# Kernel optimization log

Hardware: AMD Instinct MI355X
Metric: run time of the kernel (lower is better)

Reference implementation:

```python
import jax, jax.numpy as jnp
import numpy as np

OBS = 256      # observation_space_size == state_vector_len
SV = 2047      # STATE_VECTORS = WMG_MAX_OBS
D = 256        # tfm_vec_size = 8 heads * 32 head_size
H = 8
HD = 32
L = 2          # TFM_NUM_LAYERS
FF = 1024      # TFM_HIDDEN_SIZE
ACH = 512      # AC_HIDDEN_LAYER_SIZE
A = 16         # action_space_size


def setup_inputs() -> dict:
    key = jax.random.key(0)
    ks = jax.random.split(key, 24)
    r = lambda k, s: (jax.random.normal(k, s, jnp.float32) * 0.02)
    inp = {
        "observation": jax.random.normal(ks[0], (OBS,), jnp.float32),
        "old_vectors": jax.random.normal(ks[1], (SV, OBS), jnp.float32),
        "W_core": r(ks[2], (OBS, D)), "b_core": jnp.zeros((D,), jnp.float32),
        # memo embedding takes cat(state_vec, age_onehot) of size OBS+SV
        "W_memo": r(ks[3], (OBS + SV, D)), "b_memo": jnp.zeros((D,), jnp.float32),
        "Wq": r(ks[4], (L, D, D)), "bq": jnp.zeros((L, D), jnp.float32),
        "Wk": r(ks[5], (L, D, D)), "bk": jnp.zeros((L, D), jnp.float32),
        "Wv": r(ks[6], (L, D, D)), "bv": jnp.zeros((L, D), jnp.float32),
        "Wo": r(ks[7], (L, D, D)), "bo": jnp.zeros((L, D), jnp.float32),
        "ln1_g": jnp.ones((L, D), jnp.float32), "ln1_b": jnp.zeros((L, D), jnp.float32),
        "ln2_g": jnp.ones((L, D), jnp.float32), "ln2_b": jnp.zeros((L, D), jnp.float32),
        "W_ff1": r(ks[8], (L, D, FF)), "b_ff1": jnp.zeros((L, FF), jnp.float32),
        "W_ff2": r(ks[9], (L, FF, D)), "b_ff2": jnp.zeros((L, D), jnp.float32),
        "aW1": r(ks[10], (D, ACH)), "ab1": jnp.zeros((ACH,), jnp.float32),
        "aW2": r(ks[11], (ACH, ACH)), "ab2": jnp.zeros((ACH,), jnp.float32),
        "aWo": r(ks[12], (ACH, A)), "abo": jnp.zeros((A,), jnp.float32),
        "cW1": r(ks[13], (D, ACH)), "cb1": jnp.zeros((ACH,), jnp.float32),
        "cW2": r(ks[14], (ACH, ACH)), "cb2": jnp.zeros((ACH,), jnp.float32),
        "cWo": r(ks[15], (ACH, 1)), "cbo": jnp.zeros((1,), jnp.float32),
    }
    return inp


def _ln(x, g, b, eps=1e-5):
    m = jnp.mean(x, axis=-1, keepdims=True)
    v = jnp.mean(jnp.square(x - m), axis=-1, keepdims=True)
    return (x - m) * jax.lax.rsqrt(v + eps) * g + b


def reference(observation, old_vectors, W_core, b_core, W_memo, b_memo,
              Wq, bq, Wk, bk, Wv, bv, Wo, bo,
              ln1_g, ln1_b, ln2_g, ln2_b, W_ff1, b_ff1, W_ff2, b_ff2,
              aW1, ab1, aW2, ab2, aWo, abo, cW1, cb1, cW2, cb2, cWo, cbo):
    # core embedding [D]
    emb0 = observation @ W_core + b_core
    # fused memo + age-onehot embedding: cat(vec_i, e_i) @ W_memo == vec_i @ W_memo[:OBS] + W_memo[OBS+i]
    memo_emb = old_vectors @ W_memo[:OBS] + W_memo[OBS:] + b_memo  # [SV, D]
    x = jnp.concatenate([emb0[None, :], memo_emb], axis=0)[None]   # [1, 1+SV, D]
    S = 1 + SV
    scale = 1.0 / np.sqrt(HD).astype(np.float32)
    for l in range(L):
        q = (x @ Wq[l] + bq[l]).reshape(1, S, H, HD)
        k = (x @ Wk[l] + bk[l]).reshape(1, S, H, HD)
        v = (x @ Wv[l] + bv[l]).reshape(1, S, H, HD)
        scores = jnp.einsum('bqhd,bkhd->bhqk', q, k) * scale       # [1,H,S,S]
        probs = jax.nn.softmax(scores, axis=-1)
        ctx = jnp.einsum('bhqk,bkhd->bqhd', probs, v).reshape(1, S, D)
        x = _ln(x + ctx @ Wo[l] + bo[l], ln1_g[l], ln1_b[l])
        h = jax.nn.gelu(x @ W_ff1[l] + b_ff1[l])
        x = _ln(x + h @ W_ff2[l] + b_ff2[l], ln2_g[l], ln2_b[l])
    t = x[:, 0, :]                                                 # [1, D]
    ha = jnp.tanh(jnp.tanh(t @ aW1 + ab1) @ aW2 + ab2)
    policy = ha @ aWo + abo                                        # [1, A] logits
    hc = jnp.tanh(jnp.tanh(t @ cW1 + cb1) @ cW2 + cb2)
    value_est = hc @ cWo + cbo                                     # [1, 1]
    # WMG_MAX_MEMOS == 0 path: new state vector is tanh(observation)
    new_vector = jnp.tanh(observation)                             # [OBS]
    return value_est, policy, new_vector
```

## Files before the change

kernel.cpp:

```cpp
#include <hip/hip_runtime.h>
#include <stdint.h>

typedef __attribute__((ext_vector_type(8))) short bf16x8;
typedef __attribute__((ext_vector_type(4))) float f32x4;

constexpr int kSEQ = 2048;
constexpr int kD   = 256;
constexpr int kHD  = 32;
constexpr int kFF  = 1024;
constexpr int kA   = 16;

__device__ __forceinline__ unsigned short f2b(float f) {
  union { float f; unsigned int u; } v; v.f = f;
  unsigned int r = v.u + 0x7FFFu + ((v.u >> 16) & 1u);
  return (unsigned short)(r >> 16);
}

struct ConvTable {
  const float* src[13];
  int K[13];
  int N[13];
  int dst[13];
  int tstart[14];
};

union SharedU {
  struct { unsigned short lt[64][72]; } cv;
  struct { unsigned short Al[64][40]; unsigned short Bl[32][40]; } g64;
  struct { unsigned short Kl[64][40]; unsigned short Vt[32][72];
           unsigned short Pl[4][16][72]; } at;
  struct { unsigned short As[16][264]; float2 red[4][16]; } lg;
};

struct MegaParams {
  ConvTable tab;
  const float *obs, *oldv, *Wcore, *bcore, *Wmemo0, *bmemo, *Wmemo2;
  const float *bq, *bk, *bv, *bo, *ln1g, *ln1b, *ln2g, *ln2b, *bff1, *bff2;
  const float *aW1, *ab1, *aW2, *ab2, *aWo, *abo;
  const float *cW1, *cb1, *cW2, *cb2, *cWo, *cbo;
  float* xf; unsigned short* xb;
  unsigned short *qb, *kb, *vb, *hb, *wT;
  float *pacc, *pml, *pf, *h1, *h2, *out;
  int oQKV[2], oWoT[2], oFF1[2], oFF2[2];
  int convJobs, nsplit, tpb;
};

__device__ void conv_job(const MegaParams& p, SharedU& sh, int job) {
  const int tid = threadIdx.x;
  if (job == p.convJobs) {
    float a = p.bcore[tid];
    #pragma unroll 8
    for (int k = 0; k < 256; k++) a += p.obs[k] * p.Wcore[k * kD + tid];
    p.xf[tid] = a;
    p.xb[tid] = f2b(a);
    return;
  }
  int m = 0;
  while (job >= p.tab.tstart[m + 1]) m++;
  const int tloc = job - p.tab.tstart[m];
  const int N = p.tab.N[m], K = p.tab.K[m];
  const int ntile = N >> 6;
  const int k0 = (tloc / ntile) * 64, n0 = (tloc % ntile) * 64;
  const float* src = p.tab.src[m];
  {
    const int r = tid >> 2, c16 = (tid & 3) * 16;
    const float* sp = src + (size_t)(k0 + r) * N + n0 + c16;
    #pragma unroll
    for (int j = 0; j < 16; j++) sh.cv.lt[r][c16 + j] = f2b(sp[j]);
  }
  __syncthreads();
  {
    const int n = tid >> 2, kc = (tid & 3) * 16;
    unsigned short* dp = p.wT + p.tab.dst[m] + (size_t)(n0 + n) * K + k0 + kc;
    unsigned short g[16];
    #pragma unroll
    for (int j = 0; j < 16; j++) g[j] = sh.cv.lt[kc + j][n];
    *(bf16x8*)dp = *(bf16x8*)&g[0];
    *(bf16x8*)(dp + 8) = *(bf16x8*)&g[8];
  }
}

__device__ void memo_job(const MegaParams& p, SharedU& sh, int job) {
  const int tid = threadIdx.x;
  const int w = tid >> 6, l = tid & 63, lg = l >> 4, lr = l & 15;
  const int sr = tid >> 2, sk = (tid & 3) * 8;
  const int kr = tid >> 3, nc = (tid & 7) * 4;
  const int m0 = (job & 31) * 64, n0 = (job >> 5) * 32;
  f32x4 acc[2];
  #pragma unroll
  for (int c = 0; c < 2; c++)
    #pragma unroll
    for (int i = 0; i < 4; i++) acc[c][i] = 0.f;

  auto loadA = [&](int k0) -> bf16x8 {
    bf16x8 av;
    if (m0 + sr < 2047) {
      const float* ap = p.oldv + (size_t)(m0 + sr) * 256 + k0 + sk;
      #pragma unroll
      for (int j = 0; j < 8; j++) av[j] = (short)f2b(ap[j]);
    } else {
      #pragma unroll
      for (int j = 0; j < 8; j++) av[j] = 0;
    }
    return av;
  };
  auto loadB = [&](int k0, float* b4) {
    const float* bp = p.Wmemo0 + (size_t)(k0 + kr) * kD + n0 + nc;
    #pragma unroll
    for (int j = 0; j < 4; j++) b4[j] = bp[j];
  };

  bf16x8 av = loadA(0);
  float b4[4];
  loadB(0, b4);

  for (int k0 = 0; k0 < 256; k0 += 32) {
    __syncthreads();
    *(bf16x8*)&sh.g64.Al[sr][sk] = av;
    #pragma unroll
    for (int j = 0; j < 4; j++) sh.g64.Bl[nc + j][kr] = f2b(b4[j]);
    __syncthreads();
    if (k0 + 32 < 256) {
      av = loadA(k0 + 32);
      loadB(k0 + 32, b4);
    }
    bf16x8 af = *(bf16x8*)&sh.g64.Al[w * 16 + lr][8 * lg];
    #pragma unroll
    for (int c = 0; c < 2; c++) {
      bf16x8 bf = *(bf16x8*)&sh.g64.Bl[c * 16 + lr][8 * lg];
      acc[c] = __builtin_amdgcn_mfma_f32_16x16x32_bf16(af, bf, acc[c], 0, 0, 0);
    }
  }

  #pragma unroll
  for (int c = 0; c < 2; c++)
    #pragma unroll
    for (int i = 0; i < 4; i++) {
      const int gr = m0 + w * 16 + 4 * lg + i;
      const int gc = n0 + c * 16 + lr;
      if (gr >= 2047) continue;
      const float v = acc[c][i] + p.bmemo[gc] + p.Wmemo2[(size_t)gr * kD + gc];
      p.xf[(size_t)(gr + 1) * kD + gc] = v;
      p.xb[(size_t)(gr + 1) * kD + gc] = f2b(v);
    }
}

__global__ __launch_bounds__(256) void k_cvm(MegaParams p) {
  __shared__ SharedU sh;
  if (blockIdx.x < 256) memo_job(p, sh, blockIdx.x);
  else conv_job(p, sh, blockIdx.x - 256);
}

template <int EPI>
__device__ __forceinline__ void gemm_job(
    SharedU& sh, int m0, int n0, const unsigned short* Ap, int lda, int Kloop,
    const unsigned short* BT, int ldb,
    const float* p0, const float* p1, const float* p2,
    void* o0, void* o1, void* o2) {
  const int tid = threadIdx.x;
  const int w = tid >> 6, l = tid & 63, lg = l >> 4, lr = l & 15;
  const int sr = tid >> 2, sk = (tid & 3) * 8;
  f32x4 acc[2];
  #pragma unroll
  for (int c = 0; c < 2; c++)
    #pragma unroll
    for (int i = 0; i < 4; i++) acc[c][i] = 0.f;

  bf16x8 av = *(const bf16x8*)(Ap + (size_t)(m0 + sr) * lda + sk);
  bf16x8 bv;
  if (tid < 128) bv = *(const bf16x8*)(BT + (size_t)(n0 + sr) * ldb + sk);

  for (int k0 = 0; k0 < Kloop; k0 += 32) {
    __syncthreads();
    *(bf16x8*)&sh.g64.Al[sr][sk] = av;
    if (tid < 128) *(bf16x8*)&sh.g64.Bl[sr][sk] = bv;
    __syncthreads();
    if (k0 + 32 < Kloop) {
      av = *(const bf16x8*)(Ap + (size_t)(m0 + sr) * lda + k0 + 32 + sk);
      if (tid < 128)
        bv = *(const bf16x8*)(BT + (size_t)(n0 + sr) * ldb + k0 + 32 + sk);
    }
    bf16x8 af = *(bf16x8*)&sh.g64.Al[w * 16 + lr][8 * lg];
    #pragma unroll
    for (int c = 0; c < 2; c++) {
      bf16x8 bf = *(bf16x8*)&sh.g64.Bl[c * 16 + lr][8 * lg];
      acc[c] = __builtin_amdgcn_mfma_f32_16x16x32_bf16(af, bf, acc[c], 0, 0, 0);
    }
  }

  #pragma unroll
  for (int c = 0; c < 2; c++) {
    #pragma unroll
    for (int i = 0; i < 4; i++) {
      const int gr = m0 + w * 16 + 4 * lg + i;
      const int gc = n0 + c * 16 + lr;
      float v = acc[c][i];
      if constexpr (EPI == 1) {
        const int t = gc >> 8, cc = gc & 255;
        const float* bp = (t == 0) ? p0 : (t == 1 ? p1 : p2);
        unsigned short* op = (t == 0) ? (unsigned short*)o0
                              : (t == 1 ? (unsigned short*)o1
                                        : (unsigned short*)o2);
        v += bp[cc];
        if (t == 0) v *= 0.17677669529663687f;
        op[(size_t)gr * kD + cc] = f2b(v);
      } else if constexpr (EPI == 2) {
        v += p0[gc];
        const float u = 0.7978845608028654f * (v + 0.044715f * v * v * v);
        const float g = v / (1.0f + __expf(-2.0f * u));
        ((unsigned short*)o0)[(size_t)gr * kFF + gc] = f2b(g);
      } else {
        ((float*)o0)[(size_t)gr * kD + gc] = v;
      }
    }
  }
}

__global__ __launch_bounds__(256) void k_qkv(MegaParams p, int lyr) {
  __shared__ SharedU sh;
  const int job = blockIdx.x;
  const int m0 = (job & 31) * 64, n0 = (job >> 5) * 32;
  gemm_job<1>(sh, m0, n0, p.xb, 256, 256, p.wT + p.oQKV[lyr], 256,
              p.bq + lyr * 256, p.bk + lyr * 256, p.bv + lyr * 256,
              p.qb, p.kb, p.vb);
}

__global__ __launch_bounds__(256) void k_ff1(MegaParams p, int lyr) {
  __shared__ SharedU sh;
  const int job = blockIdx.x;
  const int m0 = (job & 31) * 64, n0 = (job >> 5) * 32;
  gemm_job<2>(sh, m0, n0, p.xb, 256, 256, p.wT + p.oFF1[lyr], 256,
              p.bff1 + lyr * 1024, nullptr, nullptr, p.hb, nullptr, nullptr);
}

__global__ __launch_bounds__(256) void k_ff2p(MegaParams p, int lyr) {
  __shared__ SharedU sh;
  const int job = blockIdx.x;
  const int m0 = (job & 31) * 64;
  const int n0 = ((job >> 5) & 7) * 32;
  const int kc = (job >> 8) * 256;
  gemm_job<3>(sh, m0, n0, p.hb + kc, kFF, 256,
              p.wT + p.oFF2[lyr] + kc, kFF, nullptr, nullptr, nullptr,
              p.pf + (size_t)(job >> 8) * kSEQ * kD, nullptr, nullptr);
}

__device__ void attn_job(SharedU& sh, int qb_, int h, int s, int tpb,
                         const unsigned short* q, const unsigned short* k,
                         const unsigned short* v, float* pacc, float* pml) {
  const int tid = threadIdx.x;
  const int w = tid >> 6, l = tid & 63, lg = l >> 4, lr = l & 15;
  const int q0 = qb_ * 64;
  const int hoff = h * kHD;
  const int sr = tid >> 2, sk = (tid & 3) * 8;
  const int t0 = s * tpb;

  const bf16x8 qf =
      *(const bf16x8*)(q + (size_t)(q0 + w * 16 + lr) * kD + hoff + 8 * lg);

  float m_[4], l_[4];
  f32x4 acc[2];
  #pragma unroll
  for (int i = 0; i < 4; i++) { m_[i] = -1e30f; l_[i] = 0.f; }
  #pragma unroll
  for (int dt = 0; dt < 2; dt++)
    #pragma unroll
    for (int i = 0; i < 4; i++) acc[dt][i] = 0.f;

  bf16x8 kreg = *(const bf16x8*)(k + (size_t)(t0 * 64 + sr) * kD + hoff + sk);
  bf16x8 vreg = *(const bf16x8*)(v + (size_t)(t0 * 64 + sr) * kD + hoff + sk);

  for (int t = 0; t < tpb; t++) {
    __syncthreads();
    *(bf16x8*)&sh.at.Kl[sr][sk] = kreg;
    #pragma unroll
    for (int j = 0; j < 8; j++) sh.at.Vt[sk + j][sr] = (unsigned short)vreg[j];
    __syncthreads();
    if (t + 1 < tpb) {
      const size_t nx = (size_t)((t0 + t + 1) * 64 + sr) * kD + hoff + sk;
      kreg = *(const bf16x8*)(k + nx);
      vreg = *(const bf16x8*)(v + nx);
    }
    f32x4 sc[4];
    #pragma unroll
    for (int c = 0; c < 4; c++) {
      f32x4 z;
      #pragma unroll
      for (int i = 0; i < 4; i++) z[i] = 0.f;
      bf16x8 kf = *(bf16x8*)&sh.at.Kl[c * 16 + lr][8 * lg];
      sc[c] = __builtin_amdgcn_mfma_f32_16x16x32_bf16(qf, kf, z, 0, 0, 0);
    }
    float tm[4];
    #pragma unroll
    for (int i = 0; i < 4; i++)
      tm[i] = fmaxf(fmaxf(sc[0][i], sc[1][i]), fmaxf(sc[2][i], sc[3][i]));
    #pragma unroll
    for (int mm = 1; mm <= 8; mm <<= 1)
      #pragma unroll
      for (int i = 0; i < 4; i++) tm[i] = fmaxf(tm[i], __shfl_xor(tm[i], mm));
    float pv[4][4], rs[4], corr[4];
    #pragma unroll
    for (int i = 0; i < 4; i++) {
      const float nm = fmaxf(m_[i], tm[i]);
      corr[i] = __expf(m_[i] - nm);
      m_[i] = nm;
      rs[i] = 0.f;
    }
    #pragma unroll
    for (int c = 0; c < 4; c++)
      #pragma unroll
      for (int i = 0; i < 4; i++) {
        pv[c][i] = __expf(sc[c][i] - m_[i]);
        rs[i] += pv[c][i];
      }
    #pragma unroll
    for (int mm = 1; mm <= 8; mm <<= 1)
      #pragma unroll
      for (int i = 0; i < 4; i++) rs[i] += __shfl_xor(rs[i], mm);
    #pragma unroll
    for (int i = 0; i < 4; i++) {
      l_[i] = l_[i] * corr[i] + rs[i];
      acc[0][i] *= corr[i];
      acc[1][i] *= corr[i];
    }
    #pragma unroll
    for (int c = 0; c < 4; c++)
      #pragma unroll
      for (int i = 0; i < 4; i++)
        sh.at.Pl[w][4 * lg + i][c * 16 + lr] = f2b(pv[c][i]);
    __syncthreads();
    #pragma unroll
    for (int k2 = 0; k2 < 2; k2++) {
      bf16x8 pf_ = *(bf16x8*)&sh.at.Pl[w][lr][k2 * 32 + 8 * lg];
      #pragma unroll
      for (int dt = 0; dt < 2; dt++) {
        bf16x8 vf = *(bf16x8*)&sh.at.Vt[dt * 16 + lr][k2 * 32 + 8 * lg];
        acc[dt] = __builtin_amdgcn_mfma_f32_16x16x32_bf16(pf_, vf, acc[dt], 0, 0, 0);
      }
    }
  }

  const int pb = s * 8 + h;
  float* pa = pacc + (size_t)pb * kSEQ * kHD;
  float* pm = pml + (size_t)pb * kSEQ * 2;
  #pragma unroll
  for (int dt = 0; dt < 2; dt++)
    #pragma unroll
    for (int i = 0; i < 4; i++) {
      const int gr = q0 + w * 16 + 4 * lg + i;
      pa[(size_t)gr * kHD + dt * 16 + lr] = acc[dt][i];
    }
  if (lr == 0) {
    #pragma unroll
    for (int i = 0; i < 4; i++) {
      const int gr = q0 + w * 16 + 4 * lg + i;
      float2 ml; ml.x = m_[i]; ml.y = l_[i];
      *(float2*)&pm[(size_t)gr * 2] = ml;
    }
  }
}

__global__ __launch_bounds__(256) void k_attn(MegaParams p) {
  __shared__ SharedU sh;
  const int job = blockIdx.x;
  const int qb_ = job & 31, h = (job >> 5) & 7, s = job >> 8;
  attn_job(sh, qb_, h, s, p.tpb, p.qb, p.kb, p.vb, p.pacc, p.pml);
}

__device__ __forceinline__ void ln_write(SharedU& sh, float vloc[4][4], int r0,
                                         const float* gam, const float* bet,
                                         float* xf, unsigned short* xb) {
  const int tid = threadIdx.x;
  const int w = tid >> 6, l = tid & 63, lg = l >> 4, lr = l & 15;
  float ps[4], ps2[4];
  #pragma unroll
  for (int i = 0; i < 4; i++) {
    ps[i] = 0.f; ps2[i] = 0.f;
    #pragma unroll
    for (int c = 0; c < 4; c++) {
      ps[i] += vloc[c][i];
      ps2[i] += vloc[c][i] * vloc[c][i];
    }
  }
  #pragma unroll
  for (int mm = 1; mm <= 8; mm <<= 1)
    #pragma unroll
    for (int i = 0; i < 4; i++) {
      ps[i] += __shfl_xor(ps[i], mm);
      ps2[i] += __shfl_xor(ps2[i], mm);
    }
  if (lr == 0) {
    #pragma unroll
    for (int i = 0; i < 4; i++) {
      float2 t; t.x = ps[i]; t.y = ps2[i];
      sh.lg.red[w][4 * lg + i] = t;
    }
  }
  __syncthreads();
  #pragma unroll
  for (int i = 0; i < 4; i++) {
    const int ri = 4 * lg + i;
    float sx = 0.f, sx2 = 0.f;
    #pragma unroll
    for (int ww = 0; ww < 4; ww++) {
      float2 t = sh.lg.red[ww][ri];
      sx += t.x; sx2 += t.y;
    }
    const float mean = sx * (1.0f / 256.0f);
    const float var = sx2 * (1.0f / 256.0f) - mean * mean;
    const float rstd = rsqrtf(var + 1e-5f);
    const int gr = r0 + ri;
    #pragma unroll
    for (int c = 0; c < 4; c++) {
      const int col = w * 64 + c * 16 + lr;
      const float y = (vloc[c][i] - mean) * rstd * gam[col] + bet[col];
      xf[(size_t)gr * kD + col] = y;
      xb[(size_t)gr * kD + col] = f2b(y);
    }
  }
}

__global__ __launch_bounds__(256) void k_woln(MegaParams p, int lyr) {
  __shared__ SharedU sh;
  const unsigned short* BT = p.wT + p.oWoT[lyr];
  const float* bias = p.bo + lyr * kD;
  const float* gam = p.ln1g + lyr * kD;
  const float* bet = p.ln1b + lyr * kD;
  const int tid = threadIdx.x;
  const int w = tid >> 6, l = tid & 63, lg = l >> 4, lr = l & 15;
  const int r0 = blockIdx.x * 16;
  {
    const int row = r0 + (tid >> 4);
    const int kc = (tid & 15) * 16;
    const int h_ = kc >> 5;
    float mx = -1e30f;
    for (int s2 = 0; s2 < p.nsplit; s2++)
      mx = fmaxf(mx, p.pml[((size_t)(s2 * 8 + h_) * kSEQ + row) * 2]);
    float L = 0.f;
    const int d0 = kc & 31;
    float o[16];
    #pragma unroll
    for (int j = 0; j < 16; j++) o[j] = 0.f;
    for (int s2 = 0; s2 < p.nsplit; s2++) {
      const size_t pb = (size_t)(s2 * 8 + h_) * kSEQ + row;
      const float2 t = *(const float2*)&p.pml[pb * 2];
      const float es = __expf(t.x - mx);
      L += t.y * es;
      const float* pa = p.pacc + pb * kHD + d0;
      #pragma unroll
      for (int j = 0; j < 16; j++) o[j] += pa[j] * es;
    }
    const float inv = 1.0f / L;
    unsigned short* dst = &sh.lg.As[tid >> 4][kc];
    #pragma unroll
    for (int j = 0; j < 16; j++) dst[j] = f2b(o[j] * inv);
  }
  __syncthreads();
  f32x4 acc[4];
  #pragma unroll
  for (int c = 0; c < 4; c++)
    #pragma unroll
    for (int i = 0; i < 4; i++) acc[c][i] = 0.f;
  #pragma unroll 2
  for (int k0 = 0; k0 < 256; k0 += 32) {
    bf16x8 af = *(bf16x8*)&sh.lg.As[lr][k0 + 8 * lg];
    #pragma unroll
    for (int c = 0; c < 4; c++) {
      bf16x8 bf = *(const bf16x8*)(BT + (size_t)(w * 64 + c * 16 + lr) * 256 +
                                   k0 + 8 * lg);
      acc[c] = __builtin_amdgcn_mfma_f32_16x16x32_bf16(af, bf, acc[c], 0, 0, 0);
    }
  }
  float vloc[4][4];
  #pragma unroll
  for (int c = 0; c < 4; c++)
    #pragma unroll
    for (int i = 0; i < 4; i++) {
      const int col = w * 64 + c * 16 + lr;
      const int gr = r0 + 4 * lg + i;
      vloc[c][i] = acc[c][i] + bias[col] + p.xf[(size_t)gr * kD + col];
    }
  ln_write(sh, vloc, r0, gam, bet, p.xf, p.xb);
}

__global__ __launch_bounds__(256) void k_ln2r(MegaParams p, int lyr) {
  const float* bias = p.bff2 + lyr * kD;
  const float* gam = p.ln2g + lyr * kD;
  const float* bet = p.ln2b + lyr * kD;
  const int w = threadIdx.x >> 6, l = threadIdx.x & 63;
  const int row = blockIdx.x * 4 + w;
  f32x4 v = *(const f32x4*)(p.xf + (size_t)row * kD + l * 4);
  f32x4 b4 = *(const f32x4*)(bias + l * 4);
  #pragma unroll
  for (int i = 0; i < 4; i++) v[i] += b4[i];
  #pragma unroll
  for (int s = 0; s < 4; s++) {
    f32x4 t = *(const f32x4*)(p.pf + ((size_t)s * kSEQ + row) * kD + l * 4);
    #pragma unroll
    for (int i = 0; i < 4; i++) v[i] += t[i];
  }
  float su = v[0] + v[1] + v[2] + v[3];
  #pragma unroll
  for (int mm = 1; mm < 64; mm <<= 1) su += __shfl_xor(su, mm);
  const float mn = su * (1.0f / 256.0f);
  const float d0 = v[0] - mn, d1 = v[1] - mn, d2 = v[2] - mn, d3 = v[3] - mn;
  float s2 = d0 * d0 + d1 * d1 + d2 * d2 + d3 * d3;
  #pragma unroll
  for (int mm = 1; mm < 64; mm <<= 1) s2 += __shfl_xor(s2, mm);
  const float rstd = rsqrtf(s2 * (1.0f / 256.0f) + 1e-5f);
  f32x4 g4 = *(const f32x4*)(gam + l * 4);
  f32x4 be4 = *(const f32x4*)(bet + l * 4);
  f32x4 y;
  y[0] = d0 * rstd * g4[0] + be4[0];
  y[1] = d1 * rstd * g4[1] + be4[1];
  y[2] = d2 * rstd * g4[2] + be4[2];
  y[3] = d3 * rstd * g4[3] + be4[3];
  *(f32x4*)(p.xf + (size_t)row * kD + l * 4) = y;
  unsigned long long pk = (unsigned long long)f2b(y[0]) |
                          ((unsigned long long)f2b(y[1]) << 16) |
                          ((unsigned long long)f2b(y[2]) << 32) |
                          ((unsigned long long)f2b(y[3]) << 48);
  *(unsigned long long*)(p.xb + (size_t)row * kD + l * 4) = pk;
}

__global__ __launch_bounds__(256) void k_h1(MegaParams p) {
  __shared__ float tl[256];
  __shared__ float red[4][64];
  const int tid = threadIdx.x;
  tl[tid] = p.xf[tid];
  __syncthreads();
  const int jj = blockIdx.x * 64;
  const bool actor = jj < 512;
  const float* W = actor ? p.aW1 : p.cW1;
  const float* b = actor ? p.ab1 : p.cb1;
  const int j0 = actor ? jj : jj - 512;
  const int ks = tid >> 6, j = tid & 63;
  float s = 0.f;
  #pragma unroll 4
  for (int k2 = ks * 64; k2 < ks * 64 + 64; k2++)
    s += tl[k2] * W[(size_t)k2 * 512 + j0 + j];
  red[ks][j] = s;
  __syncthreads();
  if (tid < 64) {
    float t = red[0][tid] + red[1][tid] + red[2][tid] + red[3][tid] + b[j0 + tid];
    p.h1[jj + tid] = tanhf(t);
  }
}

__global__ __launch_bounds__(256) void k_h2(MegaParams p) {
  __shared__ float tl[512];
  __shared__ float red[4][64];
  const int tid = threadIdx.x;
  const int jj = blockIdx.x * 64;
  const bool actor = jj < 512;
  const float* hin = actor ? p.h1 : p.h1 + 512;
  tl[tid] = hin[tid];
  tl[tid + 256] = hin[tid + 256];
  __syncthreads();
  const float* W = actor ? p.aW2 : p.cW2;
  const float* b = actor ? p.ab2 : p.cb2;
  const int j0 = actor ? jj : jj - 512;
  const int ks = tid >> 6, j = tid & 63;
  float s = 0.f;
  #pragma unroll 4
  for (int k2 = ks * 128; k2 < ks * 128 + 128; k2++)
    s += tl[k2] * W[(size_t)k2 * 512 + j0 + j];
  red[ks][j] = s;
  __syncthreads();
  if (tid < 64) {
    float t = red[0][tid] + red[1][tid] + red[2][tid] + red[3][tid] + b[j0 + tid];
    p.h2[jj + tid] = tanhf(t);
  }
}

__global__ __launch_bounds__(256) void k_h3(MegaParams p) {
  __shared__ float ha[512], hc[512], vred[4];
  const int tid = threadIdx.x;
  ha[tid] = p.h2[tid];
  ha[tid + 256] = p.h2[tid + 256];
  hc[tid] = p.h2[512 + tid];
  hc[tid + 256] = p.h2[768 + tid];
  __syncthreads();
  const int g = tid >> 4, l16 = tid & 15;
  float s = 0.f;
  for (int k2 = l16 * 32; k2 < l16 * 32 + 32; k2++)
    s += ha[k2] * p.aWo[(size_t)k2 * kA + g];
  #pragma unroll
  for (int mm = 1; mm <= 8; mm <<= 1) s += __shfl_xor(s, mm);
  if (l16 == 0) p.out[1 + g] = s + p.abo[g];
  float vv = hc[tid] * p.cWo[tid] + hc[tid + 256] * p.cWo[tid + 256];
  #pragma unroll
  for (int mm = 1; mm <= 32; mm <<= 1) vv += __shfl_xor(vv, mm);
  if ((tid & 63) == 0) vred[tid >> 6] = vv;
  __syncthreads();
  if (tid == 0)
    p.out[0] = vred[0] + vred[1] + vred[2] + vred[3] + p.cbo[0];
  p.out[17 + tid] = tanhf(p.obs[tid]);
}

extern "C" void kernel_launch(void* const* d_in, const int* in_sizes, int n_in,
                              void* d_out, int out_size, void* d_ws, size_t ws_size,
                              hipStream_t stream) {
  const float* obs   = (const float*)d_in[0];
  const float* oldv  = (const float*)d_in[1];
  const float* Wcore = (const float*)d_in[2];
  const float* bcore = (const float*)d_in[3];
  const float* Wmemo = (const float*)d_in[4];
  const float* bmemo = (const float*)d_in[5];
  const float* Wq    = (const float*)d_in[6];
  const float* bq    = (const float*)d_in[7];
  const float* Wk    = (const float*)d_in[8];
  const float* bk    = (const float*)d_in[9];
  const float* Wv    = (const float*)d_in[10];
  const float* bv    = (const float*)d_in[11];
  const float* Wo    = (const float*)d_in[12];
  const float* bo    = (const float*)d_in[13];
  const float* ln1g  = (const float*)d_in[14];
  const float* ln1b  = (const float*)d_in[15];
  const float* ln2g  = (const float*)d_in[16];
  const float* ln2b  = (const float*)d_in[17];
  const float* Wff1  = (const float*)d_in[18];
  const float* bff1  = (const float*)d_in[19];
  const float* Wff2  = (const float*)d_in[20];
  const float* bff2  = (const float*)d_in[21];

  MegaParams P;
  P.obs = obs; P.oldv = oldv; P.Wcore = Wcore; P.bcore = bcore;
  P.Wmemo0 = Wmemo; P.bmemo = bmemo; P.Wmemo2 = Wmemo + 256 * 256;
  P.bq = bq; P.bk = bk; P.bv = bv; P.bo = bo;
  P.ln1g = ln1g; P.ln1b = ln1b; P.ln2g = ln2g; P.ln2b = ln2b;
  P.bff1 = bff1; P.bff2 = bff2;
  P.aW1 = (const float*)d_in[22]; P.ab1 = (const float*)d_in[23];
  P.aW2 = (const float*)d_in[24]; P.ab2 = (const float*)d_in[25];
  P.aWo = (const float*)d_in[26]; P.abo = (const float*)d_in[27];
  P.cW1 = (const float*)d_in[28]; P.cb1 = (const float*)d_in[29];
  P.cW2 = (const float*)d_in[30]; P.cb2 = (const float*)d_in[31];
  P.cWo = (const float*)d_in[32]; P.cbo = (const float*)d_in[33];

  char* ws = (char*)d_ws;
  P.xf = (float*)(ws + 0);
  P.xb = (unsigned short*)(ws + (2u << 20));
  P.qb = (unsigned short*)(ws + (3u << 20));
  P.kb = (unsigned short*)(ws + (4u << 20));
  P.vb = (unsigned short*)(ws + (5u << 20));
  P.hb = (unsigned short*)(ws + (6u << 20));
  P.wT = (unsigned short*)(ws + (10u << 20));
  P.out = (float*)d_out;

  int nsplit = 8;
  const size_t paccOff = (size_t)14u << 20;
  const size_t pmlOff  = (size_t)31u << 20;
  const size_t pfOff   = (size_t)33u << 20;
  while (nsplit > 1 &&
         (paccOff + (size_t)nsplit * 8 * kSEQ * kHD * 4 > pmlOff ||
          pfOff + (size_t)4 * kSEQ * kD * 4 + 16384 > ws_size))
    nsplit >>= 1;
  P.pacc = (float*)(ws + paccOff);
  P.pml  = (float*)(ws + pmlOff);
  P.pf   = (float*)(ws + pfOff);
  P.h1 = (float*)(ws + pfOff + (size_t)4 * kSEQ * kD * 4);
  P.h2 = P.h1 + 1024;
  P.nsplit = nsplit;
  P.tpb = 32 / nsplit;

  int cur = 0;
  for (int l2 = 0; l2 < 2; l2++) {
    P.oQKV[l2] = cur; cur += 196608;
    P.oWoT[l2] = cur; cur += 65536;
    P.oFF1[l2] = cur; cur += 262144;
    P.oFF2[l2] = cur; cur += 262144;
  }

  int idx = 0, ts = 0;
  auto add = [&](const float* s, int K, int N, int dst) {
    P.tab.src[idx] = s; P.tab.K[idx] = K; P.tab.N[idx] = N;
    P.tab.dst[idx] = dst; P.tab.tstart[idx] = ts;
    ts += (K >> 6) * (N >> 6); idx++;
  };
  for (int l2 = 0; l2 < 2; l2++) {
    add(Wq + l2 * 65536, 256, 256, P.oQKV[l2]);
    add(Wk + l2 * 65536, 256, 256, P.oQKV[l2] + 65536);
    add(Wv + l2 * 65536, 256, 256, P.oQKV[l2] + 131072);
    add(Wo + l2 * 65536, 256, 256, P.oWoT[l2]);
    add(Wff1 + l2 * 262144, 256, 1024, P.oFF1[l2]);
    add(Wff2 + l2 * 262144, 1024, 256, P.oFF2[l2]);
  }
  P.tab.tstart[idx] = ts;
  P.convJobs = ts;

  k_cvm<<<256 + ts + 1, 256, 0, stream>>>(P);
  for (int lyr = 0; lyr < 2; lyr++) {
    k_qkv<<<768, 256, 0, stream>>>(P, lyr);
    k_attn<<<256 * nsplit, 256, 0, stream>>>(P);
    k_woln<<<128, 256, 0, stream>>>(P, lyr);
    k_ff1<<<1024, 256, 0, stream>>>(P, lyr);
    k_ff2p<<<1024, 256, 0, stream>>>(P, lyr);
    k_ln2r<<<512, 256, 0, stream>>>(P, lyr);
  }
  k_h1<<<16, 256, 0, stream>>>(P);
  k_h2<<<16, 256, 0, stream>>>(P);
  k_h3<<<1, 256, 0, stream>>>(P);
}
```

Measured before the change: 190.3 us.

## Fuse FF2 GEMM with residual LayerNorm and merge actor-critic hidden layers

Replaces the split-K FF2 GEMM, which wrote four fp32 partial buffers, and the separate LN2 reduction kernel with a single kernel. Each block stages a 16-row slice of the FF1 activations in LDS, runs the full K=1024 MFMA, adds the bias and residual, and applies LayerNorm in place. This removes the partial-sum global round trip and one launch per layer. The cost is that each block now does a long serial K loop and only 128 blocks are launched, which lowers parallelism. The actor/critic first and second MLP layers are also merged into one kernel, with each block recomputing the first layer redundantly, to save a launch.

```diff
diff --git a/kernel.cpp b/kernel.cpp
--- a/kernel.cpp
+++ b/kernel.cpp
@@ -40,7 +40,7 @@
   const float *cW1, *cb1, *cW2, *cb2, *cWo, *cbo;
   float* xf; unsigned short* xb;
   unsigned short *qb, *kb, *vb, *hb, *wT;
-  float *pacc, *pml, *pf, *h1, *h2, *out;
+  float *pacc, *pml, *h2, *out;
   int oQKV[2], oWoT[2], oFF1[2], oFF2[2];
   int convJobs, nsplit, tpb;
 };
@@ -204,13 +204,11 @@
         v += bp[cc];
         if (t == 0) v *= 0.17677669529663687f;
         op[(size_t)gr * kD + cc] = f2b(v);
-      } else if constexpr (EPI == 2) {
+      } else {
         v += p0[gc];
         const float u = 0.7978845608028654f * (v + 0.044715f * v * v * v);
         const float g = v / (1.0f + __expf(-2.0f * u));
         ((unsigned short*)o0)[(size_t)gr * kFF + gc] = f2b(g);
-      } else {
-        ((float*)o0)[(size_t)gr * kD + gc] = v;
       }
     }
   }
@@ -233,17 +231,6 @@
               p.bff1 + lyr * 1024, nullptr, nullptr, p.hb, nullptr, nullptr);
 }
 
-__global__ __launch_bounds__(256) void k_ff2p(MegaParams p, int lyr) {
-  __shared__ SharedU sh;
-  const int job = blockIdx.x;
-  const int m0 = (job & 31) * 64;
-  const int n0 = ((job >> 5) & 7) * 32;
-  const int kc = (job >> 8) * 256;
-  gemm_job<3>(sh, m0, n0, p.hb + kc, kFF, 256,
-              p.wT + p.oFF2[lyr] + kc, kFF, nullptr, nullptr, nullptr,
-              p.pf + (size_t)(job >> 8) * kSEQ * kD, nullptr, nullptr);
-}
-
 __device__ void attn_job(SharedU& sh, int qb_, int h, int s, int tpb,
                          const unsigned short* q, const unsigned short* k,
                          const unsigned short* v, float* pacc, float* pml) {
@@ -366,9 +353,10 @@
   attn_job(sh, qb_, h, s, p.tpb, p.qb, p.kb, p.vb, p.pacc, p.pml);
 }
 
-__device__ __forceinline__ void ln_write(SharedU& sh, float vloc[4][4], int r0,
-                                         const float* gam, const float* bet,
-                                         float* xf, unsigned short* xb) {
+__device__ __forceinline__ void ln_write(float2 (*red)[16], float vloc[4][4],
+                                         int r0, const float* gam,
+                                         const float* bet, float* xf,
+                                         unsigned short* xb) {
   const int tid = threadIdx.x;
   const int w = tid >> 6, l = tid & 63, lg = l >> 4, lr = l & 15;
   float ps[4], ps2[4];
@@ -392,7 +380,7 @@
     #pragma unroll
     for (int i = 0; i < 4; i++) {
       float2 t; t.x = ps[i]; t.y = ps2[i];
-      sh.lg.red[w][4 * lg + i] = t;
+      red[w][4 * lg + i] = t;
     }
   }
   __syncthreads();
@@ -402,7 +390,7 @@
     float sx = 0.f, sx2 = 0.f;
     #pragma unroll
     for (int ww = 0; ww < 4; ww++) {
-      float2 t = sh.lg.red[ww][ri];
+      float2 t = red[ww][ri];
       sx += t.x; sx2 += t.y;
     }
     const float mean = sx * (1.0f / 256.0f);
@@ -420,7 +408,8 @@
 }
 
 __global__ __launch_bounds__(256) void k_woln(MegaParams p, int lyr) {
-  __shared__ SharedU sh;
+  __shared__ unsigned short As[16][264];
+  __shared__ float2 red[4][16];
   const unsigned short* BT = p.wT + p.oWoT[lyr];
   const float* bias = p.bo + lyr * kD;
   const float* gam = p.ln1g + lyr * kD;
@@ -450,7 +439,7 @@
       for (int j = 0; j < 16; j++) o[j] += pa[j] * es;
     }
     const float inv = 1.0f / L;
-    unsigned short* dst = &sh.lg.As[tid >> 4][kc];
+    unsigned short* dst = &As[tid >> 4][kc];
     #pragma unroll
     for (int j = 0; j < 16; j++) dst[j] = f2b(o[j] * inv);
   }
@@ -462,7 +451,7 @@
     for (int i = 0; i < 4; i++) acc[c][i] = 0.f;
   #pragma unroll 2
   for (int k0 = 0; k0 < 256; k0 += 32) {
-    bf16x8 af = *(bf16x8*)&sh.lg.As[lr][k0 + 8 * lg];
+    bf16x8 af = *(bf16x8*)&As[lr][k0 + 8 * lg];
     #pragma unroll
     for (int c = 0; c < 4; c++) {
       bf16x8 bf = *(const bf16x8*)(BT + (size_t)(w * 64 + c * 16 + lr) * 256 +
@@ -479,95 +468,86 @@
       const int gr = r0 + 4 * lg + i;
       vloc[c][i] = acc[c][i] + bias[col] + p.xf[(size_t)gr * kD + col];
     }
-  ln_write(sh, vloc, r0, gam, bet, p.xf, p.xb);
-}
-
-__global__ __launch_bounds__(256) void k_ln2r(MegaParams p, int lyr) {
+  ln_write(red, vloc, r0, gam, bet, p.xf, p.xb);
+}
+
+__global__ __launch_bounds__(256) void k_ff2ln(MegaParams p, int lyr) {
+  __shared__ unsigned short As2[16][1032];
+  __shared__ float2 red[4][16];
+  const unsigned short* BT = p.wT + p.oFF2[lyr];
   const float* bias = p.bff2 + lyr * kD;
   const float* gam = p.ln2g + lyr * kD;
   const float* bet = p.ln2b + lyr * kD;
-  const int w = threadIdx.x >> 6, l = threadIdx.x & 63;
-  const int row = blockIdx.x * 4 + w;
-  f32x4 v = *(const f32x4*)(p.xf + (size_t)row * kD + l * 4);
-  f32x4 b4 = *(const f32x4*)(bias + l * 4);
-  #pragma unroll
-  for (int i = 0; i < 4; i++) v[i] += b4[i];
-  #pragma unroll
-  for (int s = 0; s < 4; s++) {
-    f32x4 t = *(const f32x4*)(p.pf + ((size_t)s * kSEQ + row) * kD + l * 4);
-    #pragma unroll
-    for (int i = 0; i < 4; i++) v[i] += t[i];
-  }
-  float su = v[0] + v[1] + v[2] + v[3];
-  #pragma unroll
-  for (int mm = 1; mm < 64; mm <<= 1) su += __shfl_xor(su, mm);
-  const float mn = su * (1.0f / 256.0f);
-  const float d0 = v[0] - mn, d1 = v[1] - mn, d2 = v[2] - mn, d3 = v[3] - mn;
-  float s2 = d0 * d0 + d1 * d1 + d2 * d2 + d3 * d3;
-  #pragma unroll
-  for (int mm = 1; mm < 64; mm <<= 1) s2 += __shfl_xor(s2, mm);
-  const float rstd = rsqrtf(s2 * (1.0f / 256.0f) + 1e-5f);
-  f32x4 g4 = *(const f32x4*)(gam + l * 4);
-  f32x4 be4 = *(const f32x4*)(bet + l * 4);
-  f32x4 y;
-  y[0] = d0 * rstd * g4[0] + be4[0];
-  y[1] = d1 * rstd * g4[1] + be4[1];
-  y[2] = d2 * rstd * g4[2] + be4[2];
-  y[3] = d3 * rstd * g4[3] + be4[3];
-  *(f32x4*)(p.xf + (size_t)row * kD + l * 4) = y;
-  unsigned long long pk = (unsigned long long)f2b(y[0]) |
-                          ((unsigned long long)f2b(y[1]) << 16) |
-                          ((unsigned long long)f2b(y[2]) << 32) |
-                          ((unsigned long long)f2b(y[3]) << 48);
-  *(unsigned long long*)(p.xb + (size_t)row * kD + l * 4) = pk;
-}
-
-__global__ __launch_bounds__(256) void k_h1(MegaParams p) {
+  const int tid = threadIdx.x;
+  const int w = tid >> 6, l = tid & 63, lg = l >> 4, lr = l & 15;
+  const int r0 = blockIdx.x * 16;
+  {
+    const int row = tid >> 4, cb = (tid & 15) * 64;
+    const unsigned short* src = p.hb + (size_t)(r0 + row) * kFF + cb;
+    #pragma unroll
+    for (int j = 0; j < 8; j++)
+      *(bf16x8*)&As2[row][cb + j * 8] = *(const bf16x8*)(src + j * 8);
+  }
+  __syncthreads();
+  f32x4 acc[4];
+  #pragma unroll
+  for (int c = 0; c < 4; c++)
+    #pragma unroll
+    for (int i = 0; i < 4; i++) acc[c][i] = 0.f;
+  #pragma unroll 4
+  for (int k0 = 0; k0 < 1024; k0 += 32) {
+    bf16x8 af = *(bf16x8*)&As2[lr][k0 + 8 * lg];
+    #pragma unroll
+    for (int c = 0; c < 4; c++) {
+      bf16x8 bf = *(const bf16x8*)(BT + (size_t)(w * 64 + c * 16 + lr) * 1024 +
+                                   k0 + 8 * lg);
+      acc[c] = __builtin_amdgcn_mfma_f32_16x16x32_bf16(af, bf, acc[c], 0, 0, 0);
+    }
+  }
+  float vloc[4][4];
+  #pragma unroll
+  for (int c = 0; c < 4; c++)
+    #pragma unroll
+    for (int i = 0; i < 4; i++) {
+      const int col = w * 64 + c * 16 + lr;
+      const int gr = r0 + 4 * lg + i;
+      vloc[c][i] = acc[c][i] + bias[col] + p.xf[(size_t)gr * kD + col];
+    }
+  ln_write(red, vloc, r0, gam, bet, p.xf, p.xb);
+}
+
+__global__ __launch_bounds__(256) void k_h12(MegaParams p) {
   __shared__ float tl[256];
+  __shared__ float hh[512];
   __shared__ float red[4][64];
   const int tid = threadIdx.x;
+  const bool actor = blockIdx.x < 8;
   tl[tid] = p.xf[tid];
   __syncthreads();
+  const float* W1 = actor ? p.aW1 : p.cW1;
+  const float* b1 = actor ? p.ab1 : p.cb1;
+  #pragma unroll
+  for (int rep = 0; rep < 2; rep++) {
+    const int j = tid + rep * 256;
+    float s = b1[j];
+    #pragma unroll 8
+    for (int k = 0; k < 256; k++) s += tl[k] * W1[(size_t)k * 512 + j];
+    hh[j] = tanhf(s);
+  }
+  __syncthreads();
+  const float* W2 = actor ? p.aW2 : p.cW2;
+  const float* b2 = actor ? p.ab2 : p.cb2;
   const int jj = blockIdx.x * 64;
-  const bool actor = jj < 512;
-  const float* W = actor ? p.aW1 : p.cW1;
-  const float* b = actor ? p.ab1 : p.cb1;
-  const int j0 = actor ? jj : jj - 512;
-  const int ks = tid >> 6, j = tid & 63;
-  float s = 0.f;
-  #pragma unroll 4
-  for (int k2 = ks * 64; k2 < ks * 64 + 64; k2++)
-    s += tl[k2] * W[(size_t)k2 * 512 + j0 + j];
-  red[ks][j] = s;
-  __syncthreads();
-  if (tid < 64) {
-    float t = red[0][tid] + red[1][tid] + red[2][tid] + red[3][tid] + b[j0 + tid];
-    p.h1[jj + tid] = tanhf(t);
-  }
-}
-
-__global__ __launch_bounds__(256) void k_h2(MegaParams p) {
-  __shared__ float tl[512];
-  __shared__ float red[4][64];
-  const int tid = threadIdx.x;
-  const int jj = blockIdx.x * 64;
-  const bool actor = jj < 512;
-  const float* hin = actor ? p.h1 : p.h1 + 512;
-  tl[tid] = hin[tid];
-  tl[tid + 256] = hin[tid + 256];
-  __syncthreads();
-  const float* W = actor ? p.aW2 : p.cW2;
-  const float* b = actor ? p.ab2 : p.cb2;
   const int j0 = actor ? jj : jj - 512;
   const int ks = tid >> 6, j = tid & 63;
   float s = 0.f;
   #pragma unroll 4
   for (int k2 = ks * 128; k2 < ks * 128 + 128; k2++)
-    s += tl[k2] * W[(size_t)k2 * 512 + j0 + j];
+    s += hh[k2] * W2[(size_t)k2 * 512 + j0 + j];
   red[ks][j] = s;
   __syncthreads();
   if (tid < 64) {
-    float t = red[0][tid] + red[1][tid] + red[2][tid] + red[3][tid] + b[j0 + tid];
+    float t = red[0][tid] + red[1][tid] + red[2][tid] + red[3][tid] + b2[j0 + tid];
     p.h2[jj + tid] = tanhf(t);
   }
 }
@@ -649,16 +629,14 @@
   int nsplit = 8;
   const size_t paccOff = (size_t)14u << 20;
   const size_t pmlOff  = (size_t)31u << 20;
-  const size_t pfOff   = (size_t)33u << 20;
+  const size_t h2Off   = (size_t)33u << 20;
   while (nsplit > 1 &&
          (paccOff + (size_t)nsplit * 8 * kSEQ * kHD * 4 > pmlOff ||
-          pfOff + (size_t)4 * kSEQ * kD * 4 + 16384 > ws_size))
+          h2Off + 16384 > ws_size))
     nsplit >>= 1;
   P.pacc = (float*)(ws + paccOff);
   P.pml  = (float*)(ws + pmlOff);
-  P.pf   = (float*)(ws + pfOff);
-  P.h1 = (float*)(ws + pfOff + (size_t)4 * kSEQ * kD * 4);
-  P.h2 = P.h1 + 1024;
+  P.h2   = (float*)(ws + h2Off);
   P.nsplit = nsplit;
   P.tpb = 32 / nsplit;
 
@@ -693,10 +671,8 @@
     k_attn<<<256 * nsplit, 256, 0, stream>>>(P);
     k_woln<<<128, 256, 0, stream>>>(P, lyr);
     k_ff1<<<1024, 256, 0, stream>>>(P, lyr);
-    k_ff2p<<<1024, 256, 0, stream>>>(P, lyr);
-    k_ln2r<<<512, 256, 0, stream>>>(P, lyr);
-  }
-  k_h1<<<16, 256, 0, stream>>>(P);
-  k_h2<<<16, 256, 0, stream>>>(P);
+    k_ff2ln<<<128, 256, 0, stream>>>(P, lyr);
+  }
+  k_h12<<<16, 256, 0, stream>>>(P);
   k_h3<<<1, 256, 0, stream>>>(P);
 }
```

Measured after the change: 223.5 us. +17.4%, slower.
